# Optimization experiments

Hardware: AMD Instinct MI355X
Metric: run time of the kernel (lower is better)

Reference implementation:

```python
import jax, jax.numpy as jnp
import numpy as np

NEG = -9e15
ALPHA = 0.2  # leaky relu slope

def setup_inputs() -> dict:
    key = jax.random.key(0)
    k1, k2, k3, k4 = jax.random.split(key, 4)
    N, Fin, Fout = 8192, 512, 256
    h = jax.random.normal(k1, (N, Fin), dtype=jnp.float32)
    adj = jax.random.randint(k2, (N, N), 0, 2, dtype=jnp.int32)
    # xavier_uniform with gain=1.414
    gain = 1.414
    limW = gain * np.sqrt(6.0 / (Fin + Fout))
    W = jax.random.uniform(k3, (Fin, Fout), dtype=jnp.float32, minval=-limW, maxval=limW)
    lima = gain * np.sqrt(6.0 / (2 * Fout + 1))
    a = jax.random.uniform(k4, (2 * Fout, 1), dtype=jnp.float32, minval=-lima, maxval=lima)
    return {"h": h, "adj": adj, "W": W, "a": a}

def reference(h, adj, W, a):
    Fout = W.shape[1]
    Wh = h @ W                                   # [N, Fout]
    # decompose a = [a1; a2]: e_ij = leaky(a1.Wh_i + a2.Wh_j)
    f1 = Wh @ a[:Fout]                           # [N, 1]
    f2 = Wh @ a[Fout:]                           # [N, 1]
    e = jax.nn.leaky_relu(f1 + f2.T, negative_slope=ALPHA)  # [N, N]
    e = jnp.where(adj > 0, e, jnp.float32(NEG))
    attention = jax.nn.softmax(e, axis=1)
    # dropout is identity at inference (training=False)
    h_prime = attention @ Wh                     # [N, Fout]
    return jax.nn.elu(h_prime)
```

## Files before the change

kernel.cpp:

```cpp
#include <hip/hip_runtime.h>
#include <cstdint>
#include <cstddef>

#define ALPHA 0.2f

typedef __attribute__((ext_vector_type(8)))  short short8;
typedef __attribute__((ext_vector_type(16))) float f32x16;

static __device__ __forceinline__ unsigned short f2bf(float x) {
  union { float f; unsigned u; } c; c.f = x;
  unsigned u = c.u;
  unsigned r = (u + 0x7FFFu + ((u >> 16) & 1u)) >> 16;
  return (unsigned short)r;
}

__global__ __launch_bounds__(256, 2) void maskgemm(const int* __restrict__ adj,
                                                   unsigned long long* __restrict__ mask,
                                                   const float* __restrict__ h,
                                                   const float* __restrict__ W,
                                                   float* __restrict__ Wh) {
  __shared__ float As[32][68];
  __shared__ float Bs[32][64];
  __shared__ unsigned long long mbuf[4][128];
  const int t = threadIdx.x;
  const int b = blockIdx.x;
  if (b % 5 == 0) {
    const int bid = b / 5;
    const int nb = bid & 3, mb = bid >> 2;
    const int m0 = mb * 64, n0 = nb * 64;
    const int ty = t >> 4, tx = t & 15;
    float acc[4][4];
#pragma unroll
    for (int i = 0; i < 4; i++)
#pragma unroll
      for (int j = 0; j < 4; j++) acc[i][j] = 0.f;

    for (int k0 = 0; k0 < 512; k0 += 32) {
#pragma unroll
      for (int c = 0; c < 2; c++) {
        int m = c * 32 + (t >> 3);
        int kq = (t & 7) * 4;
        float4 v = *(const float4*)&h[(size_t)(m0 + m) * 512 + k0 + kq];
        As[kq + 0][m] = v.x; As[kq + 1][m] = v.y;
        As[kq + 2][m] = v.z; As[kq + 3][m] = v.w;
      }
#pragma unroll
      for (int c = 0; c < 2; c++) {
        int k = c * 16 + (t >> 4);
        int n = (t & 15) * 4;
        *(float4*)&Bs[k][n] = *(const float4*)&W[(size_t)(k0 + k) * 256 + n0 + n];
      }
      __syncthreads();
#pragma unroll
      for (int k = 0; k < 32; k++) {
        float4 a = *(float4*)&As[k][ty * 4];
        float4 bb = *(float4*)&Bs[k][tx * 4];
        float av[4] = {a.x, a.y, a.z, a.w};
        float bv[4] = {bb.x, bb.y, bb.z, bb.w};
#pragma unroll
        for (int i = 0; i < 4; i++)
#pragma unroll
          for (int j = 0; j < 4; j++) acc[i][j] = fmaf(av[i], bv[j], acc[i][j]);
      }
      __syncthreads();
    }
#pragma unroll
    for (int i = 0; i < 4; i++) {
      float4 v = {acc[i][0], acc[i][1], acc[i][2], acc[i][3]};
      *(float4*)&Wh[(size_t)(m0 + ty * 4 + i) * 256 + n0 + tx * 4] = v;
    }
  } else {
    const int mask_id = b - b / 5 - 1;
    const int wave = t >> 6, lane = t & 63;
    const int row = mask_id * 4 + wave;
    const int* ap = adj + (size_t)row * 8192 + lane;
#pragma unroll 1
    for (int it0 = 0; it0 < 128; it0 += 4) {
      int a0 = ap[(it0 + 0) * 64];
      int a1 = ap[(it0 + 1) * 64];
      int a2 = ap[(it0 + 2) * 64];
      int a3 = ap[(it0 + 3) * 64];
      unsigned long long b0 = __ballot(a0 > 0);
      unsigned long long b1 = __ballot(a1 > 0);
      unsigned long long b2 = __ballot(a2 > 0);
      unsigned long long b3 = __ballot(a3 > 0);
      if (lane == 0) {
        mbuf[wave][it0 + 0] = b0; mbuf[wave][it0 + 1] = b1;
        mbuf[wave][it0 + 2] = b2; mbuf[wave][it0 + 3] = b3;
      }
    }
    __syncthreads();
    const int it = t & 127, half = t >> 7;
    const int row0 = mask_id * 4;
    unsigned long long tmp[2] = {mbuf[half * 2][it], mbuf[half * 2 + 1][it]};
    *(uint4*)&mask[(size_t)it * 8192 + row0 + half * 2] = *(const uint4*)tmp;
  }
}

__global__ __launch_bounds__(256) void rowstats(const float* __restrict__ Wh,
                                                const float* __restrict__ a,
                                                float* __restrict__ f1,
                                                float* __restrict__ f2,
                                                unsigned* __restrict__ uvpack) {
  const int t = threadIdx.x;
  const int w = t >> 6, lane = t & 63;
  const int i = blockIdx.x * 4 + w;
  float4 wv = *(const float4*)&Wh[(size_t)i * 256 + lane * 4];
  float4 a1 = *(const float4*)&a[lane * 4];
  float4 a2 = *(const float4*)&a[256 + lane * 4];
  float s1 = wv.x * a1.x + wv.y * a1.y + wv.z * a1.z + wv.w * a1.w;
  float s2 = wv.x * a2.x + wv.y * a2.y + wv.z * a2.z + wv.w * a2.w;
#pragma unroll
  for (int off = 32; off; off >>= 1) { s1 += __shfl_xor(s1, off); s2 += __shfl_xor(s2, off); }
  if (lane == 0) {
    f1[i] = s1; f2[i] = s2;
    float u = __expf(s2), v = __expf(ALPHA * s2);
    uvpack[i] = (unsigned)f2bf(u) | ((unsigned)f2bf(v) << 16);
  }
}

__global__ __launch_bounds__(256) void bpack(const float* __restrict__ Wh,
                                             unsigned short* __restrict__ BP) {
  const int t = threadIdx.x, wave = t >> 6, lane = t & 63;
  const int c32 = blockIdx.x >> 4, sblk = blockIdx.x & 15;
  const int col = c32 * 32 + (lane & 31), hi = lane >> 5;
#pragma unroll
  for (int p = 0; p < 8; p++) {
    const int s = sblk * 32 + wave * 8 + p;
    unsigned short v[8];
#pragma unroll
    for (int e = 0; e < 8; e++)
      v[e] = f2bf(Wh[(size_t)(s * 16 + hi * 8 + e) * 256 + col]);
    *(uint4*)&BP[((size_t)c32 * 512 + s) * 512 + lane * 8] = *(const uint4*)v;
  }
}

__global__ __launch_bounds__(256) void f2max_k(const float* __restrict__ f2,
                                               float* __restrict__ f2maxp) {
  __shared__ float red[256];
  const int t = threadIdx.x;
  float m = -1e30f;
  for (int c = 0; c < 32; c++) m = fmaxf(m, f2[c * 256 + t]);
  red[t] = m;
  __syncthreads();
  for (int s = 128; s; s >>= 1) {
    if (t < s) red[t] = fmaxf(red[t], red[t + s]);
    __syncthreads();
  }
  if (t == 0) f2maxp[0] = red[0];
}

#define LOADBF(BUF, SIDX)                                                        \
  {                                                                              \
    const int s_ = (SIDX) < 128 ? (SIDX) : 127;                                  \
    BUF[0] = *(const short8*)(bp0 + (size_t)(0 * 512 + s_) * 512);               \
    BUF[1] = *(const short8*)(bp0 + (size_t)(1 * 512 + s_) * 512);               \
    BUF[2] = *(const short8*)(bp0 + (size_t)(2 * 512 + s_) * 512);               \
    BUF[3] = *(const short8*)(bp0 + (size_t)(3 * 512 + s_) * 512);               \
  }

#define ATTN_SUB(KSUB, MWORD, UCA, UCB, BFC)                                     \
  {                                                                              \
    const unsigned mbyte_ = ((MWORD) >> (((KSUB) & 1) * 16 + aselsh)) & 0xFFu;   \
    const unsigned uu_[8] = {UCA.x, UCA.y, UCA.z, UCA.w, UCB.x, UCB.y, UCB.z, UCB.w}; \
    float w_[8];                                                                 \
    _Pragma("unroll")                                                            \
    for (int jj = 0; jj < 8; jj++) {                                             \
      union { unsigned u; float f; } cu_, cv_;                                   \
      cu_.u = uu_[jj] << 16;                                                     \
      cv_.u = uu_[jj] & 0xFFFF0000u;                                             \
      float wv_ = (cu_.f > Ui) ? Ai * cu_.f : Bi * cv_.f;                        \
      int ext_ = ((int)(mbyte_ << (31 - jj))) >> 31;    \
      union { float f; int i; } wu_; wu_.f = wv_; wu_.i &= ext_;                 \
      w_[jj] = wu_.f;                                                            \
    }                                                                            \
    lpriv += ((w_[0] + w_[1]) + (w_[2] + w_[3])) + ((w_[4] + w_[5]) + (w_[6] + w_[7])); \
    union { uint4 q; short8 s; } af_;                                            \
    asm("v_cvt_pk_bf16_f32 %0, %1, %2" : "=v"(af_.q.x) : "v"(w_[0]), "v"(w_[1]));\
    asm("v_cvt_pk_bf16_f32 %0, %1, %2" : "=v"(af_.q.y) : "v"(w_[2]), "v"(w_[3]));\
    asm("v_cvt_pk_bf16_f32 %0, %1, %2" : "=v"(af_.q.z) : "v"(w_[4]), "v"(w_[5]));\
    asm("v_cvt_pk_bf16_f32 %0, %1, %2" : "=v"(af_.q.w) : "v"(w_[6]), "v"(w_[7]));\
    acc[0] = __builtin_amdgcn_mfma_f32_32x32x16_bf16(af_.s, BFC[0], acc[0], 0, 0, 0); \
    acc[1] = __builtin_amdgcn_mfma_f32_32x32x16_bf16(af_.s, BFC[1], acc[1], 0, 0, 0); \
    acc[2] = __builtin_amdgcn_mfma_f32_32x32x16_bf16(af_.s, BFC[2], acc[2], 0, 0, 0); \
    acc[3] = __builtin_amdgcn_mfma_f32_32x32x16_bf16(af_.s, BFC[3], acc[3], 0, 0, 0); \
  }

#define ATTN_GROUP(G, UC, UN, MC, MN)                                            \
  {                                                                              \
    const int gn_ = (G) < 31 ? (G) + 1 : 31;                                     \
    MN = mp[(size_t)gn_ * 8192];                                                 \
    UN[0] = *(const uint4*)(uvp + gn_ * 64 + 0);                                 \
    UN[1] = *(const uint4*)(uvp + gn_ * 64 + 4);                                 \
    LOADBF(bfs2, 4 * (G) + 2);             \
    LOADBF(bfs3, 4 * (G) + 3);                                                   \
    ATTN_SUB(0, MC.x, UC[0], UC[1], bfs0);                                       \
    UN[2] = *(const uint4*)(uvp + gn_ * 64 + 16);                                \
    UN[3] = *(const uint4*)(uvp + gn_ * 64 + 20);                                \
    ATTN_SUB(1, MC.x, UC[2], UC[3], bfs1);                                       \
    UN[4] = *(const uint4*)(uvp + gn_ * 64 + 32);                                \
    UN[5] = *(const uint4*)(uvp + gn_ * 64 + 36);                                \
    LOADBF(bfs0, 4 * (G) + 4);             \
    LOADBF(bfs1, 4 * (G) + 5);                                                   \
    ATTN_SUB(2, MC.y, UC[4], UC[5], bfs2);                                       \
    UN[6] = *(const uint4*)(uvp + gn_ * 64 + 48);                                \
    UN[7] = *(const uint4*)(uvp + gn_ * 64 + 52);                                \
    ATTN_SUB(3, MC.y, UC[6], UC[7], bfs3);                                       \
  }

__global__ __launch_bounds__(256, 1) void attn_main(const unsigned long long* __restrict__ maskw,
                                                    const float* __restrict__ f1,
                                                    const unsigned* __restrict__ uvpack,
                                                    const unsigned short* __restrict__ BP,
                                                    const float* __restrict__ f2maxp,
                                                    float* __restrict__ out) {
  __shared__ float red[4][32][132];
  __shared__ float lsum[4][32];
  const int t = threadIdx.x;
  const int wave = t >> 6, lane = t & 63;
  const int jq = wave;
  const int am = lane & 31, asel = lane >> 5;
  const int aselsh = asel * 8;
  const int bid = blockIdx.x;
  const int cg = bid & 1;
  const int r0 = (bid >> 1) * 32;
  const int row = r0 + am;

  const float F2max = f2maxp[0];
  const float f1v = f1[row];
  const float x = f1v + F2max;
  const float M = x > 0.f ? x : ALPHA * x;
  const float Ai = __expf(f1v - M);
  const float Bi = __expf(ALPHA * f1v - M);
  const float Ui = __expf(-f1v);

  f32x16 acc[4] = {};
  const uint2* mp = (const uint2*)maskw + (size_t)(jq * 32) * 8192 + row;
  const unsigned* uvp = uvpack + jq * 2048 + aselsh;
  const unsigned short* bp0 = BP + ((size_t)(cg * 4) * 512 + jq * 128) * 512 + lane * 8;

  uint2 mg = mp[0], mgN;
  uint4 ug[8], ugN[8];
#pragma unroll
  for (int k = 0; k < 4; k++) {
    ug[2 * k]     = *(const uint4*)(uvp + k * 16);
    ug[2 * k + 1] = *(const uint4*)(uvp + k * 16 + 4);
  }
  short8 bfs0[4], bfs1[4], bfs2[4], bfs3[4];
  LOADBF(bfs0, 0);
  LOADBF(bfs1, 1);
  float lpriv = 0.f;

#pragma unroll 1
  for (int gg = 0; gg < 16; ++gg) {
    ATTN_GROUP(2 * gg,     ug,  ugN, mg,  mgN);
    ATTN_GROUP(2 * gg + 1, ugN, ug,  mgN, mg);
  }

#pragma unroll
  for (int ct = 0; ct < 4; ct++) {
#pragma unroll
    for (int reg = 0; reg < 16; reg++) {
      const int rowl = (reg & 3) + 8 * (reg >> 2) + 4 * asel;
      red[jq][rowl][ct * 32 + am] = acc[ct][reg];
    }
  }
  lpriv += __shfl_xor(lpriv, 32);
  if (asel == 0) lsum[jq][am] = lpriv;
  __syncthreads();

  const int rr = t >> 3, cb = (t & 7) * 16;
  const float l = lsum[0][rr] + lsum[1][rr] + lsum[2][rr] + lsum[3][rr];
  const float inv = 1.0f / fmaxf(l, 1e-30f);
#pragma unroll
  for (int cc = 0; cc < 16; cc += 4) {
    float4 v;
    v.x = red[0][rr][cb + cc + 0] + red[1][rr][cb + cc + 0] + red[2][rr][cb + cc + 0] + red[3][rr][cb + cc + 0];
    v.y = red[0][rr][cb + cc + 1] + red[1][rr][cb + cc + 1] + red[2][rr][cb + cc + 1] + red[3][rr][cb + cc + 1];
    v.z = red[0][rr][cb + cc + 2] + red[1][rr][cb + cc + 2] + red[2][rr][cb + cc + 2] + red[3][rr][cb + cc + 2];
    v.w = red[0][rr][cb + cc + 3] + red[1][rr][cb + cc + 3] + red[2][rr][cb + cc + 3] + red[3][rr][cb + cc + 3];
    v.x *= inv; v.y *= inv; v.z *= inv; v.w *= inv;
    float4 o;
    o.x = v.x > 0.f ? v.x : __expf(v.x) - 1.f;
    o.y = v.y > 0.f ? v.y : __expf(v.y) - 1.f;
    o.z = v.z > 0.f ? v.z : __expf(v.z) - 1.f;
    o.w = v.w > 0.f ? v.w : __expf(v.w) - 1.f;
    *(float4*)&out[(size_t)(r0 + rr) * 256 + cg * 128 + cb + cc] = o;
  }
}

extern "C" void kernel_launch(void* const* d_in, const int* in_sizes, int n_in,
                              void* d_out, int out_size, void* d_ws, size_t ws_size,
                              hipStream_t stream) {
  const float* h  = (const float*)d_in[0];
  const int* adj  = (const int*)d_in[1];
  const float* W  = (const float*)d_in[2];
  const float* a  = (const float*)d_in[3];
  float* out = (float*)d_out;
  char* ws = (char*)d_ws;

  float* Wh            = (float*)ws;
  unsigned long long* mask = (unsigned long long*)(ws + (size_t)(8u << 20));
  unsigned short* BP   = (unsigned short*)(ws + (size_t)(16u << 20));
  float* f1            = (float*)(ws + (size_t)(20u << 20));
  float* f2            = (float*)(ws + (size_t)(20u << 20) + (32u << 10));
  unsigned* uvpack     = (unsigned*)(ws + (size_t)(20u << 20) + (64u << 10));
  float* f2maxp        = (float*)(ws + (size_t)(20u << 20) + (96u << 10));

  maskgemm<<<2560, 256, 0, stream>>>(adj, mask, h, W, Wh);
  rowstats<<<2048, 256, 0, stream>>>(Wh, a, f1, f2, uvpack);
  bpack<<<128, 256, 0, stream>>>(Wh, BP);
  f2max_k<<<1, 256, 0, stream>>>(f2, f2maxp);
  attn_main<<<512, 256, 0, stream>>>(mask, f1, uvpack, BP, f2maxp, out);
}
```

Measured before the change: 468.9 us.

## Compute Wh with bf16 MFMA and derive f1/f2 from h·(W·a)

The fp32 SIMT tiled GEMM for Wh = h·W is replaced by a bf16 MFMA 32x32x16 path that reads a pre-packed bf16 copy of W and writes Wh as bf16. A new small kernel computes W·a1 and W·a2 and packs W, so f1 and f2 become dot products of h with those vectors and no longer depend on Wh. bpack now reads bf16 Wh, which halves its reads and drops its conversions. The intent is to cut the GEMM cost inside the fused mask/GEMM launch. The tradeoff is an extra launch and bf16 rounding of h and W before the GEMM, which adds precision error.

After: 487.2 us. +3.9%, slower.

```diff
diff --git a/kernel.cpp b/kernel.cpp
--- a/kernel.cpp
+++ b/kernel.cpp
@@ -14,63 +14,84 @@
   return (unsigned short)r;
 }
 
+__global__ __launch_bounds__(256) void wa_wpack(const float* __restrict__ W,
+                                                const float* __restrict__ a,
+                                                float* __restrict__ wa1,
+                                                float* __restrict__ wa2,
+                                                unsigned short* __restrict__ WP) {
+  const int t = threadIdx.x, b = blockIdx.x;
+  if (b < 8) {
+    __shared__ float p1[64][4], p2[64][4];
+    const int kl = t >> 2, q = t & 3;
+    const int k = b * 64 + kl;
+    float s1 = 0.f, s2 = 0.f;
+    for (int n = q * 64; n < q * 64 + 64; ++n) {
+      float wv = W[(size_t)k * 256 + n];
+      s1 += wv * a[n];
+      s2 += wv * a[256 + n];
+    }
+    p1[kl][q] = s1; p2[kl][q] = s2;
+    __syncthreads();
+    if (t < 64) {
+      wa1[b * 64 + t] = (p1[t][0] + p1[t][1]) + (p1[t][2] + p1[t][3]);
+      wa2[b * 64 + t] = (p2[t][0] + p2[t][1]) + (p2[t][2] + p2[t][3]);
+    }
+  } else {
+    const int wb = b - 8;
+    const int l = t & 63, rep = t >> 6;
+#pragma unroll
+    for (int f = 0; f < 8; ++f) {
+      const int fid = wb * 8 + f;
+      const int n32 = fid >> 5, k16 = fid & 31;
+#pragma unroll
+      for (int ee = 0; ee < 2; ++ee) {
+        const int e = rep * 2 + ee;
+        WP[((size_t)(n32 * 32 + k16) * 64 + l) * 8 + e] =
+            f2bf(W[(size_t)(k16 * 16 + (l >> 5) * 8 + e) * 256 + n32 * 32 + (l & 31)]);
+      }
+    }
+  }
+}
+
 __global__ __launch_bounds__(256, 2) void maskgemm(const int* __restrict__ adj,
                                                    unsigned long long* __restrict__ mask,
                                                    const float* __restrict__ h,
-                                                   const float* __restrict__ W,
-                                                   float* __restrict__ Wh) {
-  __shared__ float As[32][68];
-  __shared__ float Bs[32][64];
+                                                   const unsigned short* __restrict__ WP,
+                                                   unsigned short* __restrict__ whb) {
   __shared__ unsigned long long mbuf[4][128];
   const int t = threadIdx.x;
   const int b = blockIdx.x;
-  if (b % 5 == 0) {
-    const int bid = b / 5;
-    const int nb = bid & 3, mb = bid >> 2;
-    const int m0 = mb * 64, n0 = nb * 64;
-    const int ty = t >> 4, tx = t & 15;
-    float acc[4][4];
-#pragma unroll
-    for (int i = 0; i < 4; i++)
-#pragma unroll
-      for (int j = 0; j < 4; j++) acc[i][j] = 0.f;
-
-    for (int k0 = 0; k0 < 512; k0 += 32) {
-#pragma unroll
-      for (int c = 0; c < 2; c++) {
-        int m = c * 32 + (t >> 3);
-        int kq = (t & 7) * 4;
-        float4 v = *(const float4*)&h[(size_t)(m0 + m) * 512 + k0 + kq];
-        As[kq + 0][m] = v.x; As[kq + 1][m] = v.y;
-        As[kq + 2][m] = v.z; As[kq + 3][m] = v.w;
-      }
-#pragma unroll
-      for (int c = 0; c < 2; c++) {
-        int k = c * 16 + (t >> 4);
-        int n = (t & 15) * 4;
-        *(float4*)&Bs[k][n] = *(const float4*)&W[(size_t)(k0 + k) * 256 + n0 + n];
-      }
-      __syncthreads();
-#pragma unroll
-      for (int k = 0; k < 32; k++) {
-        float4 a = *(float4*)&As[k][ty * 4];
-        float4 bb = *(float4*)&Bs[k][tx * 4];
-        float av[4] = {a.x, a.y, a.z, a.w};
-        float bv[4] = {bb.x, bb.y, bb.z, bb.w};
-#pragma unroll
-        for (int i = 0; i < 4; i++)
-#pragma unroll
-          for (int j = 0; j < 4; j++) acc[i][j] = fmaf(av[i], bv[j], acc[i][j]);
-      }
-      __syncthreads();
-    }
-#pragma unroll
-    for (int i = 0; i < 4; i++) {
-      float4 v = {acc[i][0], acc[i][1], acc[i][2], acc[i][3]};
-      *(float4*)&Wh[(size_t)(m0 + ty * 4 + i) * 256 + n0 + tx * 4] = v;
+  if (b % 9 == 0) {
+    const int gid = b / 9;
+    const int m0 = gid * 32;
+    const int w = t >> 6, lane = t & 63;
+    const int am = lane & 31, asel = lane >> 5;
+    f32x16 acc0 = {}, acc1 = {};
+    const float* ap = h + (size_t)(m0 + am) * 512 + asel * 8;
+    const unsigned short* wpa = WP + ((size_t)((2 * w) * 32) * 64 + lane) * 8;
+    const unsigned short* wpb = WP + ((size_t)((2 * w + 1) * 32) * 64 + lane) * 8;
+#pragma unroll 4
+    for (int ks = 0; ks < 32; ++ks) {
+      float4 a0 = *(const float4*)(ap + ks * 16);
+      float4 a1v = *(const float4*)(ap + ks * 16 + 4);
+      union { uint4 q; short8 s; } af;
+      asm("v_cvt_pk_bf16_f32 %0, %1, %2" : "=v"(af.q.x) : "v"(a0.x), "v"(a0.y));
+      asm("v_cvt_pk_bf16_f32 %0, %1, %2" : "=v"(af.q.y) : "v"(a0.z), "v"(a0.w));
+      asm("v_cvt_pk_bf16_f32 %0, %1, %2" : "=v"(af.q.z) : "v"(a1v.x), "v"(a1v.y));
+      asm("v_cvt_pk_bf16_f32 %0, %1, %2" : "=v"(af.q.w) : "v"(a1v.z), "v"(a1v.w));
+      short8 b0 = *(const short8*)(wpa + (size_t)ks * 512);
+      short8 b1 = *(const short8*)(wpb + (size_t)ks * 512);
+      acc0 = __builtin_amdgcn_mfma_f32_32x32x16_bf16(af.s, b0, acc0, 0, 0, 0);
+      acc1 = __builtin_amdgcn_mfma_f32_32x32x16_bf16(af.s, b1, acc1, 0, 0, 0);
+    }
+#pragma unroll
+    for (int reg = 0; reg < 16; ++reg) {
+      const int rowl = (reg & 3) + 8 * (reg >> 2) + 4 * asel;
+      whb[(size_t)(m0 + rowl) * 256 + (2 * w) * 32 + am]     = f2bf(acc0[reg]);
+      whb[(size_t)(m0 + rowl) * 256 + (2 * w + 1) * 32 + am] = f2bf(acc1[reg]);
     }
   } else {
-    const int mask_id = b - b / 5 - 1;
+    const int mask_id = b - b / 9 - 1;
     const int wave = t >> 6, lane = t & 63;
     const int row = mask_id * 4 + wave;
     const int* ap = adj + (size_t)row * 8192 + lane;
@@ -97,19 +118,26 @@
   }
 }
 
-__global__ __launch_bounds__(256) void rowstats(const float* __restrict__ Wh,
-                                                const float* __restrict__ a,
-                                                float* __restrict__ f1,
-                                                float* __restrict__ f2,
-                                                unsigned* __restrict__ uvpack) {
+__global__ __launch_bounds__(256) void fvec(const float* __restrict__ h,
+                                            const float* __restrict__ wa1,
+                                            const float* __restrict__ wa2,
+                                            float* __restrict__ f1,
+                                            float* __restrict__ f2,
+                                            unsigned* __restrict__ uvpack) {
   const int t = threadIdx.x;
   const int w = t >> 6, lane = t & 63;
   const int i = blockIdx.x * 4 + w;
-  float4 wv = *(const float4*)&Wh[(size_t)i * 256 + lane * 4];
-  float4 a1 = *(const float4*)&a[lane * 4];
-  float4 a2 = *(const float4*)&a[256 + lane * 4];
-  float s1 = wv.x * a1.x + wv.y * a1.y + wv.z * a1.z + wv.w * a1.w;
-  float s2 = wv.x * a2.x + wv.y * a2.y + wv.z * a2.z + wv.w * a2.w;
+  const float* hp = h + (size_t)i * 512 + lane * 8;
+  float4 h0 = *(const float4*)hp;
+  float4 h1 = *(const float4*)(hp + 4);
+  float4 wA0 = *(const float4*)&wa1[lane * 8];
+  float4 wA1 = *(const float4*)&wa1[lane * 8 + 4];
+  float4 wB0 = *(const float4*)&wa2[lane * 8];
+  float4 wB1 = *(const float4*)&wa2[lane * 8 + 4];
+  float s1 = h0.x * wA0.x + h0.y * wA0.y + h0.z * wA0.z + h0.w * wA0.w
+           + h1.x * wA1.x + h1.y * wA1.y + h1.z * wA1.z + h1.w * wA1.w;
+  float s2 = h0.x * wB0.x + h0.y * wB0.y + h0.z * wB0.z + h0.w * wB0.w
+           + h1.x * wB1.x + h1.y * wB1.y + h1.z * wB1.z + h1.w * wB1.w;
 #pragma unroll
   for (int off = 32; off; off >>= 1) { s1 += __shfl_xor(s1, off); s2 += __shfl_xor(s2, off); }
   if (lane == 0) {
@@ -119,7 +147,7 @@
   }
 }
 
-__global__ __launch_bounds__(256) void bpack(const float* __restrict__ Wh,
+__global__ __launch_bounds__(256) void bpack(const unsigned short* __restrict__ whb,
                                              unsigned short* __restrict__ BP) {
   const int t = threadIdx.x, wave = t >> 6, lane = t & 63;
   const int c32 = blockIdx.x >> 4, sblk = blockIdx.x & 15;
@@ -130,7 +158,7 @@
     unsigned short v[8];
 #pragma unroll
     for (int e = 0; e < 8; e++)
-      v[e] = f2bf(Wh[(size_t)(s * 16 + hi * 8 + e) * 256 + col]);
+      v[e] = whb[(size_t)(s * 16 + hi * 8 + e) * 256 + col];
     *(uint4*)&BP[((size_t)c32 * 512 + s) * 512 + lane * 8] = *(const uint4*)v;
   }
 }
@@ -192,7 +220,7 @@
     MN = mp[(size_t)gn_ * 8192];                                                 \
     UN[0] = *(const uint4*)(uvp + gn_ * 64 + 0);                                 \
     UN[1] = *(const uint4*)(uvp + gn_ * 64 + 4);                                 \
-    LOADBF(bfs2, 4 * (G) + 2);             \
+    LOADBF(bfs2, 4 * (G) + 2);                                                   \
     LOADBF(bfs3, 4 * (G) + 3);                                                   \
     ATTN_SUB(0, MC.x, UC[0], UC[1], bfs0);                                       \
     UN[2] = *(const uint4*)(uvp + gn_ * 64 + 16);                                \
@@ -200,7 +228,7 @@
     ATTN_SUB(1, MC.x, UC[2], UC[3], bfs1);                                       \
     UN[4] = *(const uint4*)(uvp + gn_ * 64 + 32);                                \
     UN[5] = *(const uint4*)(uvp + gn_ * 64 + 36);                                \
-    LOADBF(bfs0, 4 * (G) + 4);             \
+    LOADBF(bfs0, 4 * (G) + 4);                                                   \
     LOADBF(bfs1, 4 * (G) + 5);                                                   \
     ATTN_SUB(2, MC.y, UC[4], UC[5], bfs2);                                       \
     UN[6] = *(const uint4*)(uvp + gn_ * 64 + 48);                                \
@@ -299,7 +327,10 @@
   float* out = (float*)d_out;
   char* ws = (char*)d_ws;
 
-  float* Wh            = (float*)ws;
+  unsigned short* whb  = (unsigned short*)ws;
+  unsigned short* WP   = (unsigned short*)(ws + (size_t)(4u << 20));
+  float* wa1           = (float*)(ws + (size_t)(5u << 20));
+  float* wa2           = (float*)(ws + (size_t)(5u << 20) + (4u << 10));
   unsigned long long* mask = (unsigned long long*)(ws + (size_t)(8u << 20));
   unsigned short* BP   = (unsigned short*)(ws + (size_t)(16u << 20));
   float* f1            = (float*)(ws + (size_t)(20u << 20));
@@ -307,9 +338,10 @@
   unsigned* uvpack     = (unsigned*)(ws + (size_t)(20u << 20) + (64u << 10));
   float* f2maxp        = (float*)(ws + (size_t)(20u << 20) + (96u << 10));
 
-  maskgemm<<<2560, 256, 0, stream>>>(adj, mask, h, W, Wh);
-  rowstats<<<2048, 256, 0, stream>>>(Wh, a, f1, f2, uvpack);
-  bpack<<<128, 256, 0, stream>>>(Wh, BP);
+  wa_wpack<<<40, 256, 0, stream>>>(W, a, wa1, wa2, WP);
+  maskgemm<<<2304, 256, 0, stream>>>(adj, mask, h, WP, whb);
+  fvec<<<2048, 256, 0, stream>>>(h, wa1, wa2, f1, f2, uvpack);
+  bpack<<<128, 256, 0, stream>>>(whb, BP);
   f2max_k<<<1, 256, 0, stream>>>(f2, f2maxp);
   attn_main<<<512, 256, 0, stream>>>(mask, f1, uvpack, BP, f2maxp, out);
 }
```
